# Kernel tuning notes

Measured on AMD Instinct MI355X. Metric: run time of the kernel, lower is better.

Reference implementation:

```python
import jax, jax.numpy as jnp
import numpy as np

B, C, H, W = 2, 64, 256, 256
P = 3          # n_pyramids
NO = 16        # per-pyramid output channels
FEX = P * NO   # 48
N = 32768      # |yi| = mask.sum()


def _conv(x, w):
    return jax.lax.conv_general_dilated(
        x, w, window_strides=(1, 1), padding='SAME',
        dimension_numbers=('NCHW', 'OIHW', 'NCHW'))


def _mask_weight(mask):
    # MaskedConv: w = mask / clamp(avg3x3(mask), 1e-8)  (computed under no_grad)
    avg = jnp.ones((1, 1, 3, 3), mask.dtype) / 9.0
    wm = _conv(mask, avg)
    return jax.lax.stop_gradient(mask / jnp.clip(wm, 1e-8))


def _mconv(x, w, wm):
    return _conv(x, w) * wm


def _resblock(x, w1, w2, mask, wm):
    x = mask * x
    r = jax.nn.relu(_mconv(x, w1, wm))
    r = _mconv(r, w2, wm)
    return x + r


def setup_inputs() -> dict:
    key = jax.random.key(0)
    ks = jax.random.split(key, 12)
    rng = np.random.default_rng(0)
    yi_np = np.sort(rng.choice(H * W, size=N, replace=False)).astype(np.int32)
    mask_flat = np.zeros(H * W, np.float32)
    mask_flat[yi_np] = 1.0
    mask = jnp.asarray(mask_flat).reshape(1, 1, H, W)
    # near-identity homography (3x3)
    m = jnp.asarray(np.array([[0.9, 0.05, 2.0],
                              [-0.03, 1.1, -1.0],
                              [1e-4, -2e-4, 1.0]], np.float32))
    s = 0.05
    return {
        'xs': jax.random.normal(ks[0], (P, B, C, H, W), jnp.float32),
        'mask': mask,
        'yi': jnp.asarray(yi_np),
        'm': m,
        'ss_res_w': s * jax.random.normal(ks[1], (P, 2, 2, C, C, 3, 3), jnp.float32),
        'ss_out_w': s * jax.random.normal(ks[2], (P, NO, C, 3, 3), jnp.float32),
        'feat_res_w': s * jax.random.normal(ks[3], (2, 2, FEX, FEX, 3, 3), jnp.float32),
        'samp_w1': s * jax.random.normal(ks[4], (FEX, FEX + 1), jnp.float32),
        'samp_b1': s * jax.random.normal(ks[5], (FEX,), jnp.float32),
        'samp_w2': s * jax.random.normal(ks[6], (FEX, FEX), jnp.float32),
        'samp_b2': s * jax.random.normal(ks[7], (FEX,), jnp.float32),
        'samp_w3': s * jax.random.normal(ks[8], (P, FEX), jnp.float32),
        'samp_b3': s * jax.random.normal(ks[9], (P,), jnp.float32),
    }


def reference(xs, mask, yi, m, ss_res_w, ss_out_w, feat_res_w,
              samp_w1, samp_b1, samp_w2, samp_b2, samp_w3, samp_b3):
    wm = _mask_weight(mask)
    # ---- MSResFeature: per-pyramid MaskedResSeq(64->64->16, depth=3) ----
    feats = []
    for i in range(P):  # small fixed loop over pyramids
        x = mask * xs[i]
        x = _resblock(x, ss_res_w[i, 0, 0], ss_res_w[i, 0, 1], mask, wm)
        x = _resblock(x, ss_res_w[i, 1, 0], ss_res_w[i, 1, 1], mask, wm)
        x = _mconv(x, ss_out_w[i], wm)
        feats.append(x)
    f = jnp.concatenate(feats, axis=1)  # (B, 48, H, W)
    # shared trunk: MaskedResSeq(48->48->48, depth=3), residual
    g = mask * f
    g = _resblock(g, feat_res_w[0, 0], feat_res_w[0, 1], mask, wm)
    g = _resblock(g, feat_res_w[1, 0], feat_res_w[1, 1], mask, wm)
    f = f + g
    b = f.shape[0]
    # ---- gather at sparse indices yi ----
    ff = f.reshape(b, FEX, -1)[:, :, yi]  # (B, 48, N)
    # ---- dsda: |Jacobian det| of projective warp, log-scaled (no_grad) ----
    ygrid, xgrid = jnp.meshgrid(jnp.arange(H, dtype=f.dtype),
                                jnp.arange(W, dtype=f.dtype), indexing='ij')
    wcoord = m[2, 0] * xgrid + m[2, 1] * ygrid + m[2, 2]
    dsda = jnp.abs(jnp.linalg.det(m)) / jnp.clip(jnp.abs(wcoord), 1e-8) ** 3
    dsda = jnp.log(dsda.reshape(-1)[yi] + 1e-8)
    dsda = jax.lax.stop_gradient(jnp.broadcast_to(dsda[None, None, :], (b, 1, N)))
    h = jnp.concatenate((ff, dsda), axis=1)  # (B, 49, N)
    # ---- 1x1 Conv1d sampler MLP ----
    h = jax.nn.relu(jnp.einsum('oc,bcn->bon', samp_w1, h) + samp_b1[None, :, None])
    h = jax.nn.relu(jnp.einsum('oc,bcn->bon', samp_w2, h) + samp_b2[None, :, None])
    p = jnp.einsum('oc,bcn->bon', samp_w3, h) + samp_b3[None, :, None]  # (B, 3, N)
    # ---- scatter back to dense grid and blend pyramids ----
    ws = jnp.zeros((b, P, H * W), f.dtype).at[:, :, yi].set(p)
    ws = ws.reshape(b, P, H, W)
    out = jnp.sum(ws.transpose(1, 0, 2, 3)[:, :, None] * xs, axis=0)  # (B, C, H, W)
    return out
```

## Files before the change

kernel.cpp:

```cpp
#include <hip/hip_runtime.h>
#include <hip/hip_bf16.h>

typedef unsigned short ushort_t;
typedef __attribute__((ext_vector_type(8))) short short8;
typedef __attribute__((ext_vector_type(4))) short short4v;
typedef __attribute__((ext_vector_type(4))) float f32x4;

constexpr int Hh = 256, Ww = 256, HW = Hh * Ww;
constexpr int Bb = 2, Cc = 64, Pp = 3, NOo = 16, FEXc = 48, Nn = 32768;
constexpr int TW = 32, TH = 8;
constexpr int HALOP = (TH + 2) * 34;
constexpr int AROWS = 352;
constexpr int PADH = 72;

__device__ inline ushort_t f2bf(float v) {
    __hip_bfloat16 h = __float2bfloat16(v);
    return *(ushort_t*)&h;
}
__device__ inline float bf2f(ushort_t u) {
    __hip_bfloat16 h = *(__hip_bfloat16*)&u;
    return __bfloat162float(h);
}
__device__ inline void gload_lds16(const ushort_t* g, ushort_t* l) {
    __builtin_amdgcn_global_load_lds(
        (const __attribute__((address_space(1))) unsigned int*)g,
        (__attribute__((address_space(3))) unsigned int*)l, 16, 0, 0);
}

__global__ __launch_bounds__(256) void k_wm(const float* __restrict__ mask,
                                            float* __restrict__ wm,
                                            float* __restrict__ zpage) {
    int pos = blockIdx.x * 256 + threadIdx.x;
    if (blockIdx.x == 0 && threadIdx.x < 64) zpage[threadIdx.x] = 0.f;
    int h = pos >> 8, w = pos & 255;
    float s = 0.f;
    #pragma unroll
    for (int dy = -1; dy <= 1; ++dy)
        #pragma unroll
        for (int dx = -1; dx <= 1; ++dx) {
            int hh = h + dy, ww = w + dx;
            if (hh >= 0 && hh < Hh && ww >= 0 && ww < Ww) s += mask[hh * Ww + ww];
        }
    float avg = s * (1.f / 9.f);
    wm[pos] = mask[pos] / fmaxf(avg, 1e-8f);
}

__global__ __launch_bounds__(256) void k_zero(float4* __restrict__ p) {
    p[blockIdx.x * 256 + threadIdx.x] = make_float4(0.f, 0.f, 0.f, 0.f);
}

__global__ __launch_bounds__(256) void k_wx_res(const float* __restrict__ src,
                                                ushort_t* __restrict__ dst) {
    int idx = blockIdx.x * 256 + threadIdx.x;
    int j = idx / 36864; int rem = idx - j * 36864;
    int t = rem >> 12; int o = (rem >> 6) & 63; int c = rem & 63;
    dst[idx] = f2bf(src[j * 36864 + o * 576 + c * 9 + t]);
}
__global__ __launch_bounds__(256) void k_wx_out(const float* __restrict__ src,
                                                ushort_t* __restrict__ dst) {
    int idx = blockIdx.x * 256 + threadIdx.x;
    int i = idx / 9216; int rem = idx - i * 9216;
    int t = rem >> 10; int o = (rem >> 6) & 15; int c = rem & 63;
    dst[idx] = f2bf(src[i * 9216 + o * 576 + c * 9 + t]);
}
__global__ __launch_bounds__(256) void k_wx_trunk(const float* __restrict__ src,
                                                  ushort_t* __restrict__ dst) {
    int idx = blockIdx.x * 256 + threadIdx.x;
    int j = idx / 27648; int rem = idx - j * 27648;
    int t = rem / 3072; int rem2 = rem - t * 3072;
    int o = rem2 >> 6; int c = rem2 & 63;
    float v = (c < 48) ? src[j * (48 * 48 * 9) + o * 432 + c * 9 + t] : 0.f;
    dst[idx] = f2bf(v);
}
__global__ __launch_bounds__(256) void k_wx_mlp(
    const float* __restrict__ w1, const float* __restrict__ b1,
    const float* __restrict__ w2, const float* __restrict__ b2,
    const float* __restrict__ w3, const float* __restrict__ b3,
    ushort_t* __restrict__ dst) {
    int idx = blockIdx.x * 256 + threadIdx.x;
    float v = 0.f;
    if (idx < 3072) {
        int o = idx >> 6, c = idx & 63;
        v = (c < 49) ? w1[o * 49 + c] : (c == 49 ? b1[o] : 0.f);
    } else if (idx < 6144) {
        int o = (idx - 3072) >> 6, c = idx & 63;
        v = (c < 48) ? w2[o * 48 + c] : (c == 48 ? b2[o] : 0.f);
    } else {
        int o = (idx - 6144) >> 6, c = idx & 63;
        if (o < 3) v = (c < 48) ? w3[o * 48 + c] : (c == 49 ? b3[o] : 0.f);
    }
    dst[idx] = f2bf(v);
}

__global__ __launch_bounds__(256) void k_xm(const float* __restrict__ xs,
                                            const float* __restrict__ mask,
                                            ushort_t* __restrict__ X) {
    __shared__ float l[64 * 65];
    const int p0 = blockIdx.x * 64;
    const size_t zoff = (size_t)blockIdx.y * 64 * HW;
    const int tid = threadIdx.x;
    const int px = tid & 63;
    const float mv = mask[p0 + px];
    #pragma unroll
    for (int k = 0; k < 16; ++k) {
        int c = (tid >> 6) + 4 * k;
        l[c * 65 + px] = xs[zoff + (size_t)c * HW + p0 + px] * mv;
    }
    __syncthreads();
    #pragma unroll
    for (int k = 0; k < 2; ++k) {
        int idx = tid + k * 256;
        int p = idx >> 3, c8 = idx & 7;
        short8 v;
        #pragma unroll
        for (int i = 0; i < 8; ++i) v[i] = (short)f2bf(l[(c8 * 8 + i) * 65 + p]);
        *(short8*)&X[zoff + (size_t)(p0 + p) * 64 + c8 * 8] = v;
    }
}

template <int OC, int MODE, bool TOF>
__global__ __launch_bounds__(256) void k_mconv(
    const ushort_t* __restrict__ in,
    const ushort_t* __restrict__ wgt, int wstride,
    const float* __restrict__ wm,
    const ushort_t* __restrict__ zp,
    const ushort_t* __restrict__ base,
    ushort_t* __restrict__ out) {
    constexpr int NM = OC / 16;
    constexpr int WROWS = 9 * OC;
    constexpr int WDMA = WROWS / 16;
    extern __shared__ __align__(1024) ushort_t smem[];
    ushort_t* alds = smem;
    ushort_t* wlds = smem + AROWS * 64;
    const int tid = threadIdx.x;
    const int wv = tid >> 6;
    const int ln = tid & 63;
    const int w0 = blockIdx.x * TW, h0 = blockIdx.y * TH;
    const int zz = blockIdx.z;
    const ushort_t* inb = in + (size_t)zz * HW * 64;
    const ushort_t* wB = wgt + (size_t)(zz >> 1) * wstride;
    const ushort_t* baseb = base ? base + (size_t)zz * HW * 64 : nullptr;
    ushort_t* outb = TOF ? out + (size_t)(zz & 1) * HW * 64 : out + (size_t)zz * HW * 64;
    const int ocb = TOF ? (zz >> 1) * 16 : 0;

    const int lo = ln & 15, slr = ln >> 4, g8 = slr * 8;

    f32x4 acc[NM][4];
    #pragma unroll
    for (int mf = 0; mf < NM; ++mf)
        #pragma unroll
        for (int nf = 0; nf < 4; ++nf) acc[mf][nf] = (f32x4){0.f, 0.f, 0.f, 0.f};

    #pragma unroll
    for (int k = 0; k < 11; ++k) {
        int s = wv * 11 + k;
        int pp = s * 8 + (ln >> 3);
        int r = (pp * 241) >> 13;
        int col = pp - r * 34;
        int gh = h0 + r - 1, gw = w0 + col - 1;
        bool ok = (pp < HALOP) & (gh >= 0) & (gh < Hh) & (gw >= 0) & (gw < Ww);
        int che = ((ln & 7) ^ (pp & 7)) << 3;
        const ushort_t* src = ok ? inb + (size_t)(gh * Ww + gw) * 64 + che : zp + che;
        gload_lds16(src, &alds[s * 512]);
    }

    #pragma unroll
    for (int h = 0; h < 2; ++h) {
        if (h) __syncthreads();
        #pragma unroll
        for (int k = 0; k < (WDMA + 3) / 4; ++k) {
            int s = wv + 4 * k;
            if (s < WDMA) {
                int r = s * 16 + (ln >> 2);
                int d = ln & 3;
                int j = d ^ ((r ^ (r >> 2)) & 3);
                gload_lds16(wB + (size_t)r * 64 + h * 32 + j * 8, &wlds[s * 512]);
            }
        }
        asm volatile("s_waitcnt vmcnt(0)" ::: "memory");
        __syncthreads();

        #pragma unroll
        for (int dy = 0; dy < 3; ++dy)
            #pragma unroll
            for (int dx = 0; dx < 3; ++dx) {
                const int t = dy * 3 + dx;
                short8 bfr[4];
                #pragma unroll
                for (int nf = 0; nf < 4; ++nf) {
                    int pp2 = (2 * wv + (nf >> 1) + dy) * 34 + (nf & 1) * 16 + lo + dx;
                    bfr[nf] = *(const short8*)
                        &alds[pp2 * 64 + (((h * 4 + slr) ^ (pp2 & 7)) << 3)];
                }
                short8 afr[NM];
                #pragma unroll
                for (int mf = 0; mf < NM; ++mf) {
                    int r = t * OC + mf * 16 + lo;
                    afr[mf] = *(const short8*)
                        &wlds[r * 32 + ((slr ^ ((r ^ (r >> 2)) & 3)) << 3)];
                }
                #pragma unroll
                for (int mf = 0; mf < NM; ++mf)
                    #pragma unroll
                    for (int nf = 0; nf < 4; ++nf)
                        acc[mf][nf] = __builtin_amdgcn_mfma_f32_16x16x32_bf16(
                            afr[mf], bfr[nf], acc[mf][nf], 0, 0, 0);
            }
    }

    #pragma unroll
    for (int nf = 0; nf < 4; ++nf) {
        int r = h0 + 2 * wv + (nf >> 1);
        int x = w0 + (nf & 1) * 16 + lo;
        int pos = r * Ww + x;
        float wmv = wm[pos];
        #pragma unroll
        for (int mf = 0; mf < NM; ++mf) {
            int o0 = ocb + mf * 16 + slr * 4;
            size_t oi = (size_t)pos * 64 + o0;
            float v[4];
            #pragma unroll
            for (int j = 0; j < 4; ++j) v[j] = acc[mf][nf][j] * wmv;
            if (MODE == 0) {
                #pragma unroll
                for (int j = 0; j < 4; ++j) v[j] = fmaxf(v[j], 0.f);
            } else if (MODE == 1) {
                short4v bv = *(const short4v*)&baseb[oi];
                #pragma unroll
                for (int j = 0; j < 4; ++j) v[j] += bf2f((ushort_t)bv[j]);
            }
            short4v sv;
            #pragma unroll
            for (int j = 0; j < 4; ++j) sv[j] = (short)f2bf(v[j]);
            *(short4v*)&outb[oi] = sv;
        }
    }
}

__global__ __launch_bounds__(256) void k_gather_mlp(
    const ushort_t* __restrict__ F, const ushort_t* __restrict__ G,
    const int* __restrict__ yi, const float* __restrict__ m,
    const ushort_t* __restrict__ wA1, const ushort_t* __restrict__ wA2,
    const ushort_t* __restrict__ wA3, float* __restrict__ pvd) {
    __shared__ __align__(16) ushort_t HA[4 * 16 * PADH];
    __shared__ __align__(16) ushort_t HB[4 * 16 * PADH];
    const int tid = threadIdx.x, wv = tid >> 6, ln = tid & 63;
    ushort_t* ha = HA + wv * 16 * PADH;
    ushort_t* hb = HB + wv * 16 * PADH;
    const int t0 = blockIdx.x * 64 + wv * 16;
    const int b = t0 >> 15;
    const int lo = ln & 15, g8 = (ln >> 4) * 8;

    #pragma unroll
    for (int rnd = 0; rnd < 2; ++rnd) {
        int j = rnd * 64 + ln;
        if (j < 96) {
            int pt = j / 6, sl = j - pt * 6;
            int n = (t0 + pt) & (Nn - 1);
            int pos = yi[n];
            size_t gi = ((size_t)(b * HW) + pos) * 64 + sl * 8;
            short8 fa = *(const short8*)&F[gi];
            short8 ga = *(const short8*)&G[gi];
            short8 sv;
            #pragma unroll
            for (int i = 0; i < 8; ++i)
                sv[i] = (short)f2bf(bf2f((ushort_t)fa[i]) + bf2f((ushort_t)ga[i]));
            *(short8*)&ha[pt * PADH + sl * 8] = sv;
        }
    }
    if (ln < 16) {
        int pt = ln;
        int n = (t0 + pt) & (Nn - 1);
        int pos = yi[n];
        float det = m[0] * (m[4] * m[8] - m[5] * m[7])
                  - m[1] * (m[3] * m[8] - m[5] * m[6])
                  + m[2] * (m[3] * m[7] - m[4] * m[6]);
        int yr = pos >> 8, xc = pos & 255;
        float wc = m[6] * (float)xc + m[7] * (float)yr + m[8];
        float cw = fmaxf(fabsf(wc), 1e-8f);
        float dsda = fabsf(det) / (cw * cw * cw);
        float ld = logf(dsda + 1e-8f);
        const ushort_t one = f2bf(1.0f);
        short8 z = {0, 0, 0, 0, 0, 0, 0, 0};
        short8 sa = z; sa[0] = (short)f2bf(ld); sa[1] = (short)one;
        short8 sb = z; sb[0] = (short)one;
        *(short8*)&ha[pt * PADH + 48] = sa;
        *(short8*)&ha[pt * PADH + 56] = z;
        *(short8*)&hb[pt * PADH + 48] = sb;
        *(short8*)&hb[pt * PADH + 56] = z;
    }
    asm volatile("s_waitcnt lgkmcnt(0)" ::: "memory");

    f32x4 a1[3] = {{0.f,0.f,0.f,0.f},{0.f,0.f,0.f,0.f},{0.f,0.f,0.f,0.f}};
    #pragma unroll
    for (int ks = 0; ks < 2; ++ks) {
        short8 bf = *(const short8*)&ha[lo * PADH + ks * 32 + g8];
        #pragma unroll
        for (int mf = 0; mf < 3; ++mf) {
            short8 af = *(const short8*)&wA1[(mf * 16 + lo) * 64 + ks * 32 + g8];
            a1[mf] = __builtin_amdgcn_mfma_f32_16x16x32_bf16(af, bf, a1[mf], 0, 0, 0);
        }
    }
    #pragma unroll
    for (int mf = 0; mf < 3; ++mf) {
        short4v sv;
        #pragma unroll
        for (int j = 0; j < 4; ++j) sv[j] = (short)f2bf(fmaxf(a1[mf][j], 0.f));
        *(short4v*)&hb[lo * PADH + mf * 16 + (ln >> 4) * 4] = sv;
    }
    asm volatile("s_waitcnt lgkmcnt(0)" ::: "memory");

    f32x4 a2[3] = {{0.f,0.f,0.f,0.f},{0.f,0.f,0.f,0.f},{0.f,0.f,0.f,0.f}};
    #pragma unroll
    for (int ks = 0; ks < 2; ++ks) {
        short8 bf = *(const short8*)&hb[lo * PADH + ks * 32 + g8];
        #pragma unroll
        for (int mf = 0; mf < 3; ++mf) {
            short8 af = *(const short8*)&wA2[(mf * 16 + lo) * 64 + ks * 32 + g8];
            a2[mf] = __builtin_amdgcn_mfma_f32_16x16x32_bf16(af, bf, a2[mf], 0, 0, 0);
        }
    }
    #pragma unroll
    for (int mf = 0; mf < 3; ++mf) {
        short4v sv;
        #pragma unroll
        for (int j = 0; j < 4; ++j) sv[j] = (short)f2bf(fmaxf(a2[mf][j], 0.f));
        *(short4v*)&ha[lo * PADH + mf * 16 + (ln >> 4) * 4] = sv;
    }
    asm volatile("s_waitcnt lgkmcnt(0)" ::: "memory");

    f32x4 a3 = {0.f, 0.f, 0.f, 0.f};
    #pragma unroll
    for (int ks = 0; ks < 2; ++ks) {
        short8 bf = *(const short8*)&ha[lo * PADH + ks * 32 + g8];
        short8 af = *(const short8*)&wA3[lo * 64 + ks * 32 + g8];
        a3 = __builtin_amdgcn_mfma_f32_16x16x32_bf16(af, bf, a3, 0, 0, 0);
    }
    if (ln < 16) {
        int n = (t0 + lo) & (Nn - 1);
        int pos = yi[n];
        #pragma unroll
        for (int j = 0; j < 3; ++j)
            pvd[(size_t)(b * Pp + j) * HW + pos] = a3[j];
    }
}

__global__ __launch_bounds__(256) void k_blend(const float4* __restrict__ xs,
                                               const float4* __restrict__ pvd,
                                               float4* __restrict__ out) {
    int i = blockIdx.x * 256 + threadIdx.x;
    int pos4 = i & (HW / 4 - 1);
    int bc = i >> 14;
    int b = bc >> 6;
    float4 acc = make_float4(0.f, 0.f, 0.f, 0.f);
    #pragma unroll
    for (int p = 0; p < Pp; ++p) {
        float4 pv = pvd[(b * Pp + p) * (HW / 4) + pos4];
        float4 x = xs[p * (Bb * Cc * HW / 4) + i];
        acc.x += pv.x * x.x;
        acc.y += pv.y * x.y;
        acc.z += pv.z * x.z;
        acc.w += pv.w * x.w;
    }
    out[i] = acc;
}

extern "C" void kernel_launch(void* const* d_in, const int* in_sizes, int n_in,
                              void* d_out, int out_size, void* d_ws, size_t ws_size,
                              hipStream_t stream) {
    const float* xs        = (const float*)d_in[0];
    const float* mask      = (const float*)d_in[1];
    const int*   yi        = (const int*)d_in[2];
    const float* m         = (const float*)d_in[3];
    const float* ss_res_w  = (const float*)d_in[4];
    const float* ss_out_w  = (const float*)d_in[5];
    const float* feat_res_w= (const float*)d_in[6];
    const float* w1 = (const float*)d_in[7];
    const float* b1 = (const float*)d_in[8];
    const float* w2 = (const float*)d_in[9];
    const float* b2 = (const float*)d_in[10];
    const float* w3 = (const float*)d_in[11];
    const float* b3 = (const float*)d_in[12];

    float* wm    = (float*)d_ws;
    float* zpage = wm + HW;
    float* pvd   = zpage + 64;
    ushort_t* wB = (ushort_t*)(pvd + (size_t)Bb * Pp * HW);
    constexpr size_t RES_T = 12 * 9 * 64 * 64;
    constexpr size_t OUT_T = 3 * 9 * 16 * 64;
    constexpr size_t TRK_T = 4 * 9 * 48 * 64;
    constexpr size_t MLP_T = 7168;
    constexpr size_t ZT = (size_t)Pp * Bb * HW * 64;
    ushort_t* wA = wB + RES_T + OUT_T + TRK_T;
    ushort_t* X = wA + MLP_T;
    ushort_t* U = X + ZT;
    ushort_t* V = U + ZT;
    ushort_t* F = V + ZT;
    ushort_t* G = F + (size_t)Bb * HW * 64;
    const ushort_t* zp = (const ushort_t*)zpage;

    k_wm<<<HW / 256, 256, 0, stream>>>(mask, wm, zpage);
    k_wx_res  <<<RES_T / 256, 256, 0, stream>>>(ss_res_w, wB);
    k_wx_out  <<<OUT_T / 256, 256, 0, stream>>>(ss_out_w, wB + RES_T);
    k_wx_trunk<<<TRK_T / 256, 256, 0, stream>>>(feat_res_w, wB + RES_T + OUT_T);
    k_wx_mlp  <<<MLP_T / 256, 256, 0, stream>>>(w1, b1, w2, b2, w3, b3, wA);

    const dim3 gridP(Ww / TW, Hh / TH, Pp * Bb);
    const dim3 gridT(Ww / TW, Hh / TH, Bb);
    const int RS = 4 * 9 * 64 * 64;
    const int OS = 9 * 16 * 64;
    constexpr size_t SH64 = (size_t)AROWS * 128 + 9 * 64 * 64;
    constexpr size_t SH48 = (size_t)AROWS * 128 + 9 * 48 * 64;
    constexpr size_t SH16 = (size_t)AROWS * 128 + 9 * 16 * 64;

    k_xm<<<dim3(HW / 64, Pp * Bb), 256, 0, stream>>>(xs, mask, X);
    k_mconv<64, 0, false><<<gridP, 256, SH64, stream>>>(X, wB,             RS, wm, zp, nullptr, U);
    k_mconv<64, 1, false><<<gridP, 256, SH64, stream>>>(U, wB + 1 * 36864, RS, wm, zp, X,       V);
    k_mconv<64, 0, false><<<gridP, 256, SH64, stream>>>(V, wB + 2 * 36864, RS, wm, zp, nullptr, U);
    k_mconv<64, 1, false><<<gridP, 256, SH64, stream>>>(U, wB + 3 * 36864, RS, wm, zp, V,       V);
    k_mconv<16, 2, true ><<<gridP, 256, SH16, stream>>>(V, wB + RES_T,     OS, wm, zp, nullptr, F);

    const ushort_t* tw = wB + RES_T + OUT_T;
    k_mconv<48, 0, false><<<gridT, 256, SH48, stream>>>(F, tw,             0, wm, zp, nullptr, U);
    k_mconv<48, 1, false><<<gridT, 256, SH48, stream>>>(U, tw + 1 * 27648, 0, wm, zp, F,       G);
    k_mconv<48, 0, false><<<gridT, 256, SH48, stream>>>(G, tw + 2 * 27648, 0, wm, zp, nullptr, U);
    k_mconv<48, 1, false><<<gridT, 256, SH48, stream>>>(U, tw + 3 * 27648, 0, wm, zp, G,       G);

    k_zero<<<(Bb * Pp * HW / 4) / 256, 256, 0, stream>>>((float4*)pvd);
    k_gather_mlp<<<Bb * Nn / 64, 256, 0, stream>>>(F, G, yi, m,
        wA, wA + 3072, wA + 6144, pvd);
    k_blend<<<(Bb * Cc * HW / 4) / 256, 256, 0, stream>>>((const float4*)xs, (const float4*)pvd,
                                                          (float4*)d_out);
}
```

Before: 324.5 us.

## Fuse each residual block's two masked convs into one kernel with halo recompute

Adds a k_pair kernel that runs both 3x3 masked convolutions of a residual block in one launch. It loads a 2-pixel halo tile, computes the intermediate ReLU activation for the extended region, and keeps it in LDS, so the intermediate tensor never goes through global memory. Weights are staged in two 32-channel halves to fit LDS. This replaces four launches with two for both the pyramid and trunk stages, at the cost of halo recomputation and more LDS per block, which may lower occupancy.

```diff
diff --git a/kernel.cpp b/kernel.cpp
--- a/kernel.cpp
+++ b/kernel.cpp
@@ -11,6 +11,7 @@
 constexpr int TW = 32, TH = 8;
 constexpr int HALOP = (TH + 2) * 34;
 constexpr int AROWS = 352;
+constexpr int PROWS = 432;
 constexpr int PADH = 72;
 
 __device__ inline ushort_t f2bf(float v) {
@@ -115,6 +116,220 @@
         #pragma unroll
         for (int i = 0; i < 8; ++i) v[i] = (short)f2bf(l[(c8 * 8 + i) * 65 + p]);
         *(short8*)&X[zoff + (size_t)(p0 + p) * 64 + c8 * 8] = v;
+    }
+}
+
+template <int OC, int MODE>
+__global__ __launch_bounds__(256) void k_pair(
+    const ushort_t* __restrict__ in,
+    const ushort_t* __restrict__ wgt, int wstride,
+    const float* __restrict__ wm,
+    const ushort_t* __restrict__ zp,
+    const ushort_t* __restrict__ fb,
+    ushort_t* __restrict__ out) {
+    constexpr int NM = OC / 16;
+    constexpr int WROWS = 9 * OC;
+    constexpr int WDMA = WROWS / 16;
+    constexpr int C2OFF = 9 * OC * 64;
+    extern __shared__ __align__(1024) ushort_t smem[];
+    ushort_t* alds = smem;
+    ushort_t* mlds = smem;
+    ushort_t* wlds = smem + PROWS * 64;
+    const int tid = threadIdx.x, wv = tid >> 6, ln = tid & 63;
+    const int lo = ln & 15, slr = ln >> 4;
+    const int w0 = blockIdx.x * TW, h0 = blockIdx.y * TH;
+    const int zz = blockIdx.z;
+    const ushort_t* inb = in + (size_t)zz * HW * 64;
+    ushort_t* outb = out + (size_t)zz * HW * 64;
+    const ushort_t* wg1 = wgt + (size_t)(zz >> 1) * wstride;
+
+    auto wstage = [&](const ushort_t* ws, int ck) {
+        #pragma unroll
+        for (int k = 0; k < (WDMA + 3) / 4; ++k) {
+            int s = wv + 4 * k;
+            if (s < WDMA) {
+                int r = s * 16 + (ln >> 2);
+                int d = ln & 3;
+                int j = d ^ ((r ^ (r >> 2)) & 3);
+                gload_lds16(ws + (size_t)r * 64 + ck * 32 + j * 8, &wlds[s * 512]);
+            }
+        }
+    };
+
+    #pragma unroll
+    for (int k = 0; k < 14; ++k) {
+        int s = 4 * k + wv;
+        if (s < 54) {
+            int pp = s * 8 + (ln >> 3);
+            int r = (pp * 228) >> 13;
+            int col = pp - r * 36;
+            int gh = h0 + r - 2, gw = w0 + col - 2;
+            bool ok = (gh >= 0) & (gh < Hh) & (gw >= 0) & (gw < Ww);
+            int che = ((ln & 7) ^ (pp & 7)) << 3;
+            const ushort_t* src = ok ? inb + (size_t)(gh * Ww + gw) * 64 + che : zp + che;
+            gload_lds16(src, &alds[s * 512]);
+        }
+    }
+    wstage(wg1, 0);
+    asm volatile("s_waitcnt vmcnt(0)" ::: "memory");
+    __syncthreads();
+
+    const int rb = (wv < 3) ? wv * 3 : 8;
+    const int nr = (wv < 2) ? 3 : 2;
+    f32x4 a1[NM][3][3];
+    #pragma unroll
+    for (int mf = 0; mf < NM; ++mf)
+        #pragma unroll
+        for (int j = 0; j < 3; ++j)
+            #pragma unroll
+            for (int cf = 0; cf < 3; ++cf) a1[mf][j][cf] = (f32x4){0.f, 0.f, 0.f, 0.f};
+
+    #pragma unroll
+    for (int h = 0; h < 2; ++h) {
+        if (h) {
+            __syncthreads();
+            wstage(wg1, 1);
+            asm volatile("s_waitcnt vmcnt(0)" ::: "memory");
+            __syncthreads();
+        }
+        #pragma unroll
+        for (int dy = 0; dy < 3; ++dy)
+            #pragma unroll
+            for (int dx = 0; dx < 3; ++dx) {
+                const int t = dy * 3 + dx;
+                short8 af[NM];
+                #pragma unroll
+                for (int mf = 0; mf < NM; ++mf) {
+                    int r = t * OC + mf * 16 + lo;
+                    af[mf] = *(const short8*)&wlds[r * 32 + ((slr ^ ((r ^ (r >> 2)) & 3)) << 3)];
+                }
+                #pragma unroll
+                for (int j = 0; j < 3; ++j) if (j < nr) {
+                    #pragma unroll
+                    for (int cf = 0; cf < 3; ++cf) {
+                        int cc = cf * 16 + lo + dx;
+                        if (cf == 2) cc = min(cc, 35);
+                        int pp2 = (rb + j + dy) * 36 + cc;
+                        short8 b = *(const short8*)&alds[pp2 * 64 + (((h * 4 + slr) ^ (pp2 & 7)) << 3)];
+                        #pragma unroll
+                        for (int mf = 0; mf < NM; ++mf)
+                            a1[mf][j][cf] = __builtin_amdgcn_mfma_f32_16x16x32_bf16(
+                                af[mf], b, a1[mf][j][cf], 0, 0, 0);
+                    }
+                }
+            }
+    }
+
+    short4v bres[4][NM];
+    #pragma unroll
+    for (int nf = 0; nf < 4; ++nf) {
+        int ppb = (2 * wv + (nf >> 1) + 2) * 36 + (nf & 1) * 16 + lo + 2;
+        #pragma unroll
+        for (int mf = 0; mf < NM; ++mf) {
+            int o0 = mf * 16 + slr * 4;
+            bres[nf][mf] = *(const short4v*)
+                &alds[ppb * 64 + (((o0 >> 3) ^ (ppb & 7)) << 3) + (slr & 1) * 4];
+        }
+    }
+    __syncthreads();
+
+    #pragma unroll
+    for (int j = 0; j < 3; ++j) if (j < nr) {
+        int mr = rb + j;
+        #pragma unroll
+        for (int cf = 0; cf < 3; ++cf) {
+            int mc = cf * 16 + lo;
+            if (mc < 34) {
+                int gh = h0 + mr - 1, gw = w0 + mc - 1;
+                bool ok = (gh >= 0) & (gh < Hh) & (gw >= 0) & (gw < Ww);
+                float wmv = ok ? wm[gh * Ww + gw] : 0.f;
+                int mpx = mr * 34 + mc;
+                #pragma unroll
+                for (int mf = 0; mf < NM; ++mf) {
+                    int o0 = mf * 16 + slr * 4;
+                    short4v sv;
+                    #pragma unroll
+                    for (int q = 0; q < 4; ++q)
+                        sv[q] = (short)f2bf(fmaxf(a1[mf][j][cf][q] * wmv, 0.f));
+                    *(short4v*)&mlds[mpx * 64 + (((o0 >> 3) ^ (mpx & 7)) << 3) + (slr & 1) * 4] = sv;
+                }
+                if (OC < 64) {
+                    int o0 = 48 + slr * 4;
+                    short4v zv = {0, 0, 0, 0};
+                    *(short4v*)&mlds[mpx * 64 + (((o0 >> 3) ^ (mpx & 7)) << 3) + (slr & 1) * 4] = zv;
+                }
+            }
+        }
+    }
+    __syncthreads();
+    wstage(wg1 + C2OFF, 0);
+    asm volatile("s_waitcnt vmcnt(0)" ::: "memory");
+    __syncthreads();
+
+    f32x4 a2[NM][4];
+    #pragma unroll
+    for (int mf = 0; mf < NM; ++mf)
+        #pragma unroll
+        for (int nf = 0; nf < 4; ++nf) a2[mf][nf] = (f32x4){0.f, 0.f, 0.f, 0.f};
+
+    #pragma unroll
+    for (int h = 0; h < 2; ++h) {
+        if (h) {
+            __syncthreads();
+            wstage(wg1 + C2OFF, 1);
+            asm volatile("s_waitcnt vmcnt(0)" ::: "memory");
+            __syncthreads();
+        }
+        #pragma unroll
+        for (int dy = 0; dy < 3; ++dy)
+            #pragma unroll
+            for (int dx = 0; dx < 3; ++dx) {
+                const int t = dy * 3 + dx;
+                short8 af[NM];
+                #pragma unroll
+                for (int mf = 0; mf < NM; ++mf) {
+                    int r = t * OC + mf * 16 + lo;
+                    af[mf] = *(const short8*)&wlds[r * 32 + ((slr ^ ((r ^ (r >> 2)) & 3)) << 3)];
+                }
+                short8 bfr[4];
+                #pragma unroll
+                for (int nf = 0; nf < 4; ++nf) {
+                    int pp2 = (2 * wv + (nf >> 1) + dy) * 34 + (nf & 1) * 16 + lo + dx;
+                    bfr[nf] = *(const short8*)&mlds[pp2 * 64 + (((h * 4 + slr) ^ (pp2 & 7)) << 3)];
+                }
+                #pragma unroll
+                for (int mf = 0; mf < NM; ++mf)
+                    #pragma unroll
+                    for (int nf = 0; nf < 4; ++nf)
+                        a2[mf][nf] = __builtin_amdgcn_mfma_f32_16x16x32_bf16(
+                            af[mf], bfr[nf], a2[mf][nf], 0, 0, 0);
+            }
+    }
+
+    #pragma unroll
+    for (int nf = 0; nf < 4; ++nf) {
+        int r = h0 + 2 * wv + (nf >> 1);
+        int x = w0 + (nf & 1) * 16 + lo;
+        int pos = r * Ww + x;
+        float wmv = wm[pos];
+        #pragma unroll
+        for (int mf = 0; mf < NM; ++mf) {
+            int o0 = mf * 16 + slr * 4;
+            size_t oi = (size_t)pos * 64 + o0;
+            float v[4];
+            #pragma unroll
+            for (int q = 0; q < 4; ++q)
+                v[q] = a2[mf][nf][q] * wmv + bf2f((ushort_t)bres[nf][mf][q]);
+            if (MODE == 1) {
+                short4v fv = *(const short4v*)&fb[(size_t)zz * HW * 64 + oi];
+                #pragma unroll
+                for (int q = 0; q < 4; ++q) v[q] += bf2f((ushort_t)fv[q]);
+            }
+            short4v sv;
+            #pragma unroll
+            for (int q = 0; q < 4; ++q) sv[q] = (short)f2bf(v[q]);
+            *(short4v*)&outb[oi] = sv;
+        }
     }
 }
 
@@ -409,22 +624,17 @@
     const dim3 gridT(Ww / TW, Hh / TH, Bb);
     const int RS = 4 * 9 * 64 * 64;
     const int OS = 9 * 16 * 64;
-    constexpr size_t SH64 = (size_t)AROWS * 128 + 9 * 64 * 64;
-    constexpr size_t SH48 = (size_t)AROWS * 128 + 9 * 48 * 64;
-    constexpr size_t SH16 = (size_t)AROWS * 128 + 9 * 16 * 64;
+    constexpr size_t PSH64 = (size_t)(PROWS * 64 + 9 * 64 * 32) * 2;
+    constexpr size_t PSH48 = (size_t)(PROWS * 64 + 9 * 48 * 32) * 2;
+    constexpr size_t SH16  = (size_t)AROWS * 128 + 9 * 16 * 64;
 
     k_xm<<<dim3(HW / 64, Pp * Bb), 256, 0, stream>>>(xs, mask, X);
-    k_mconv<64, 0, false><<<gridP, 256, SH64, stream>>>(X, wB,             RS, wm, zp, nullptr, U);
-    k_mconv<64, 1, false><<<gridP, 256, SH64, stream>>>(U, wB + 1 * 36864, RS, wm, zp, X,       V);
-    k_mconv<64, 0, false><<<gridP, 256, SH64, stream>>>(V, wB + 2 * 36864, RS, wm, zp, nullptr, U);
-    k_mconv<64, 1, false><<<gridP, 256, SH64, stream>>>(U, wB + 3 * 36864, RS, wm, zp, V,       V);
-    k_mconv<16, 2, true ><<<gridP, 256, SH16, stream>>>(V, wB + RES_T,     OS, wm, zp, nullptr, F);
-
+    k_pair<64, 0><<<gridP, 256, PSH64, stream>>>(X, wB,             RS, wm, zp, nullptr, V);
+    k_pair<64, 0><<<gridP, 256, PSH64, stream>>>(V, wB + 2 * 36864, RS, wm, zp, nullptr, U);
+    k_mconv<16, 2, true><<<gridP, 256, SH16, stream>>>(U, wB + RES_T, OS, wm, zp, nullptr, F);
     const ushort_t* tw = wB + RES_T + OUT_T;
-    k_mconv<48, 0, false><<<gridT, 256, SH48, stream>>>(F, tw,             0, wm, zp, nullptr, U);
-    k_mconv<48, 1, false><<<gridT, 256, SH48, stream>>>(U, tw + 1 * 27648, 0, wm, zp, F,       G);
-    k_mconv<48, 0, false><<<gridT, 256, SH48, stream>>>(G, tw + 2 * 27648, 0, wm, zp, nullptr, U);
-    k_mconv<48, 1, false><<<gridT, 256, SH48, stream>>>(U, tw + 3 * 27648, 0, wm, zp, G,       G);
+    k_pair<48, 0><<<gridT, 256, PSH48, stream>>>(F, tw,             0, wm, zp, nullptr, U);
+    k_pair<48, 0><<<gridT, 256, PSH48, stream>>>(U, tw + 2 * 27648, 0, wm, zp, nullptr, G);
 
     k_zero<<<(Bb * Pp * HW / 4) / 256, 256, 0, stream>>>((float4*)pvd);
     k_gather_mlp<<<Bb * Nn / 64, 256, 0, stream>>>(F, G, yi, m,
```

New measurement: 389.3 us. 1.2x slower.
